# Kernel tuning notes

Hardware: AMD Instinct MI355X
Metric: run time of the kernel (lower is better)

## Reference

```python
import jax, jax.numpy as jnp
import numpy as np

N, IN_DIM, H, L, NH, LAT = 4096, 16, 128, 4, 8, 16
HD = H // NH
FF = 2 * H
DR_THR = 0.2
LN_EPS = 1e-5


def _ln(x, s, b):
    m = x.mean(-1, keepdims=True)
    v = ((x - m) ** 2).mean(-1, keepdims=True)
    return (x - m) * jax.lax.rsqrt(v + LN_EPS) * s + b


def compute_dr_mask(x_raw):
    eta = x_raw[:, 1] * (2.62 - (-2.62)) + (-2.62)
    phi = x_raw[:, 2] * (3.1416 - (-3.1416)) + (-3.1416)
    deta = eta[:, None] - eta[None, :]
    dphi = phi[:, None] - phi[None, :]
    dphi = jnp.arctan2(jnp.sin(dphi), jnp.cos(dphi))
    dr = jnp.sqrt(deta ** 2 + dphi ** 2)
    return jnp.where(dr <= DR_THR, 0.0, -jnp.inf).astype(jnp.float32)


def setup_inputs() -> dict:
    key = jax.random.key(0)
    ks = jax.random.split(key, 32)
    g = lambda i, shape, s=0.02: (jax.random.normal(ks[i], shape, dtype=jnp.float32) * s)
    inp = {
        'x_raw': jax.random.uniform(ks[0], (N, IN_DIM), dtype=jnp.float32),
        'batch': jnp.zeros((N,), dtype=jnp.int64) if jax.config.read('jax_enable_x64') else jnp.zeros((N,), dtype=jnp.int32),
        'in_w': g(1, (H, IN_DIM), 0.1), 'in_b': jnp.zeros((H,), jnp.float32),
        'ln1_s': jnp.ones((L, H), jnp.float32), 'ln1_b': jnp.zeros((L, H), jnp.float32),
        'qkv_w': g(2, (L, 3 * H, H)), 'qkv_b': jnp.zeros((L, 3 * H), jnp.float32),
        'ao_w': g(3, (L, H, H)), 'ao_b': jnp.zeros((L, H), jnp.float32),
        'ln2_s': jnp.ones((L, H), jnp.float32), 'ln2_b': jnp.zeros((L, H), jnp.float32),
        'f1_w': g(4, (L, FF, H)), 'f1_b': jnp.zeros((L, FF), jnp.float32),
        'f2_w': g(5, (L, H, FF)), 'f2_b': jnp.zeros((L, H), jnp.float32),
        'lat1_w': g(6, (H, H), 0.08), 'lat1_b': jnp.zeros((H,), jnp.float32),
        'lat2_w': g(7, (LAT, H), 0.08), 'lat2_b': jnp.zeros((LAT,), jnp.float32),
        'b1_w': g(8, (H // 2, H), 0.08), 'b1_b': jnp.zeros((H // 2,), jnp.float32),
        'b2_w': g(9, (1, H // 2), 0.008), 'b2_b': jnp.full((1,), -3.0, jnp.float32),
    }
    return inp


def reference(x_raw, batch, in_w, in_b, ln1_s, ln1_b, qkv_w, qkv_b, ao_w, ao_b,
              ln2_s, ln2_b, f1_w, f1_b, f2_w, f2_b,
              lat1_w, lat1_b, lat2_w, lat2_b, b1_w, b1_b, b2_w, b2_b):
    mask = jax.lax.stop_gradient(compute_dr_mask(x_raw))  # [N, N] additive mask
    x = x_raw @ in_w.T + in_b  # [N, H]
    scale = 1.0 / jnp.sqrt(jnp.float32(HD))
    for l in range(L):  # norm_first TransformerEncoderLayer, eval mode (no dropout)
        h = _ln(x, ln1_s[l], ln1_b[l])
        qkv = h @ qkv_w[l].T + qkv_b[l]
        q, k, v = [t.reshape(N, NH, HD) for t in jnp.split(qkv, 3, axis=-1)]
        scores = jnp.einsum('qhd,khd->hqk', q, k) * scale + mask[None]
        attn = jax.nn.softmax(scores, axis=-1)
        o = jnp.einsum('hqk,khd->qhd', attn, v).reshape(N, H)
        x = x + o @ ao_w[l].T + ao_b[l]
        h2 = _ln(x, ln2_s[l], ln2_b[l])
        x = x + jax.nn.relu(h2 @ f1_w[l].T + f1_b[l]) @ f2_w[l].T + f2_b[l]
    lat = jax.nn.relu(x @ lat1_w.T + lat1_b) @ lat2_w.T + lat2_b  # [N, LAT]
    lat = lat / jnp.maximum(jnp.linalg.norm(lat, axis=-1, keepdims=True), 1e-12)
    beta = jax.nn.sigmoid(jax.nn.relu(x @ b1_w.T + b1_b) @ b2_w.T + b2_b)
    beta = jnp.clip(beta, 1e-6, 1 - 1e-6)  # [N, 1]
    return beta, lat
```

## Files before the change

kernel.cpp:

```cpp
#include <hip/hip_runtime.h>
#include <hip/hip_bf16.h>

typedef unsigned short u16;
typedef short short8_t __attribute__((ext_vector_type(8)));
typedef float floatx4 __attribute__((ext_vector_type(4)));

constexpr int NT = 4096, H = 128, CAP = 64;
constexpr int GRID = 256, BLK = 512, GSTRIDE = GRID * BLK;

constexpr int OFF_QKV  = 0;
constexpr int OFF_AO   = 196608;
constexpr int OFF_F1   = 262144;
constexpr int OFF_F2   = 393216;
constexpr int OFF_LAT1 = 524288;
constexpr int OFF_B1   = 540672;
constexpr int OFF_LAT2 = 548864;
constexpr int W_TOTAL  = 550912;

__device__ __forceinline__ float bfu(u16 u) { return __uint_as_float(((unsigned)u) << 16); }
__device__ __forceinline__ u16 f2bf(float f) {
  unsigned u = __float_as_uint(f);
  u += 0x7fffu + ((u >> 16) & 1u);
  return (u16)(u >> 16);
}
__device__ __forceinline__ void unpack8(uint4 u, float* f) {
  f[0] = __uint_as_float(u.x << 16); f[1] = __uint_as_float(u.x & 0xffff0000u);
  f[2] = __uint_as_float(u.y << 16); f[3] = __uint_as_float(u.y & 0xffff0000u);
  f[4] = __uint_as_float(u.z << 16); f[5] = __uint_as_float(u.z & 0xffff0000u);
  f[6] = __uint_as_float(u.w << 16); f[7] = __uint_as_float(u.w & 0xffff0000u);
}
__device__ __forceinline__ short8_t cvt8(const float* bp) {
  const float4 f0 = *(const float4*)bp, f1 = *(const float4*)(bp + 4);
  short8_t r;
  r[0] = (short)f2bf(f0.x); r[1] = (short)f2bf(f0.y);
  r[2] = (short)f2bf(f0.z); r[3] = (short)f2bf(f0.w);
  r[4] = (short)f2bf(f1.x); r[5] = (short)f2bf(f1.y);
  r[6] = (short)f2bf(f1.z); r[7] = (short)f2bf(f1.w);
  return r;
}

struct Prm {
  const float *xr, *in_w, *in_b, *ln1_s, *ln1_b, *qkv_w, *qkv_b, *ao_w, *ao_b,
              *ln2_s, *ln2_b, *f1_w, *f1_b, *f2_w, *f2_b, *lat1_w, *lat1_b,
              *lat2_w, *lat2_b, *b1_w, *b1_b, *b2_w, *b2_b;
  u16* W; u16* QKV0; u16* QKV1; float* Xg; int* NI; int* NC; float* out;
};

__global__ __launch_bounds__(BLK, 2) void prep_kernel(Prm p) {
  const int t = threadIdx.x, bid = blockIdx.x;
  const int lane = t & 63, w = t >> 6;
  const int lr = lane & 15, quad = lane >> 4;
  const int gtid = bid * BLK + t;
  const int r0 = bid * 16;
  const floatx4 FZ = {0.f, 0.f, 0.f, 0.f};

  __shared__ float Xs[16][132];
  __shared__ union {
    unsigned long long words[8][64];
    struct { u16 A16[16][152]; } g;
    u16 QS[16][384];
  } sm;

  for (int i = 49152 + gtid; i < W_TOTAL; i += GSTRIDE) {
    float v;
    if      (i < OFF_AO)   v = p.qkv_w[i];
    else if (i < OFF_F1)   v = p.ao_w[i - OFF_AO];
    else if (i < OFF_F2)   v = p.f1_w[i - OFF_F1];
    else if (i < OFF_LAT1) v = p.f2_w[i - OFF_F2];
    else if (i < OFF_B1)   v = p.lat1_w[i - OFF_LAT1];
    else if (i < OFF_LAT2) v = p.b1_w[i - OFF_B1];
    else                   v = p.lat2_w[i - OFF_LAT2];
    p.W[i] = f2bf(v);
  }
  for (int i = t; i < 16 * H; i += BLK) {
    const int r = i >> 7, c = i & 127;
    const float* xp = p.xr + (size_t)(r0 + r) * 16;
    const float* wp = p.in_w + c * 16;
    float acc = p.in_b[c];
#pragma unroll
    for (int k = 0; k < 16; ++k) acc += xp[k] * wp[k];
    Xs[r][c] = acc;
    p.Xg[(size_t)(r0 + r) * H + c] = acc;
  }
  for (int uu = 0; uu < 2; ++uu) {
    const int q0 = r0 + uu * 8;
    double qe[8], qp_[8];
#pragma unroll
    for (int j = 0; j < 8; ++j) {
      qe[j]  = (double)p.xr[(q0 + j) * 16 + 1] * 5.24 - 2.62;
      qp_[j] = (double)p.xr[(q0 + j) * 16 + 2] * 6.2832 - 3.1416;
    }
    for (int c = 0; c < 8; ++c) {
      const int k = c * 512 + t;
      const double ke = (double)p.xr[k * 16 + 1] * 5.24 - 2.62;
      const double kp = (double)p.xr[k * 16 + 2] * 6.2832 - 3.1416;
#pragma unroll
      for (int j = 0; j < 8; ++j) {
        const double de = qe[j] - ke;
        double dp = qp_[j] - kp;
        dp -= 6.283185307179586 * rint(dp * 0.15915494309189535);
        const unsigned long long bm = __ballot((de * de + dp * dp) <= 0.04);
        if (lane == 0) sm.words[j][c * 8 + w] = bm;
      }
    }
    __syncthreads();
    {
      unsigned long long m = sm.words[w][lane];
      const int cnt = __popcll(m);
      int incl = cnt;
#pragma unroll
      for (int off = 1; off < 64; off <<= 1) {
        const int n = __shfl_up(incl, off);
        if (lane >= off) incl += n;
      }
      int pos = incl - cnt;
      const int qq = q0 + w;
      const int kbase = (lane >> 3) * 512 + (lane & 7) * 64;
      while (m) {
        const int b = __builtin_ctzll(m);
        m &= m - 1;
        if (pos < CAP) p.NI[qq * CAP + pos] = kbase + b;
        ++pos;
      }
      if (lane == 63) p.NC[qq] = incl > CAP ? CAP : incl;
    }
    __syncthreads();
  }
  {
    const int r = t >> 5, j0 = (t & 31) * 4;
    const float4 xv = *(const float4*)&Xs[r][j0];
    float v0 = xv.x, v1 = xv.y, v2 = xv.z, v3 = xv.w;
    float s = v0 + v1 + v2 + v3;
    float ss = v0 * v0 + v1 * v1 + v2 * v2 + v3 * v3;
#pragma unroll
    for (int off = 1; off <= 16; off <<= 1) {
      s += __shfl_xor(s, off); ss += __shfl_xor(ss, off);
    }
    const float mean = s * (1.f / 128.f);
    const float rstd = rsqrtf(ss * (1.f / 128.f) - mean * mean + 1e-5f);
    v0 = (v0 - mean) * rstd * p.ln1_s[j0]     + p.ln1_b[j0];
    v1 = (v1 - mean) * rstd * p.ln1_s[j0 + 1] + p.ln1_b[j0 + 1];
    v2 = (v2 - mean) * rstd * p.ln1_s[j0 + 2] + p.ln1_b[j0 + 2];
    v3 = (v3 - mean) * rstd * p.ln1_s[j0 + 3] + p.ln1_b[j0 + 3];
    uint2 pk;
    pk.x = (unsigned)f2bf(v0) | ((unsigned)f2bf(v1) << 16);
    pk.y = (unsigned)f2bf(v2) | ((unsigned)f2bf(v3) << 16);
    *(uint2*)&sm.g.A16[r][j0] = pk;
  }
  __syncthreads();
  {
    const int c0 = w * 48;
    floatx4 a0 = FZ, a1 = FZ, a2 = FZ;
#pragma unroll
    for (int k0 = 0; k0 < 128; k0 += 32) {
      short8_t a  = *(const short8_t*)&sm.g.A16[lr][k0 + quad * 8];
      short8_t b0 = cvt8(&p.qkv_w[(size_t)(c0 + lr) * 128 + k0 + quad * 8]);
      short8_t b1 = cvt8(&p.qkv_w[(size_t)(c0 + 16 + lr) * 128 + k0 + quad * 8]);
      short8_t b2 = cvt8(&p.qkv_w[(size_t)(c0 + 32 + lr) * 128 + k0 + quad * 8]);
      a0 = __builtin_amdgcn_mfma_f32_16x16x32_bf16(a, b0, a0, 0, 0, 0);
      a1 = __builtin_amdgcn_mfma_f32_16x16x32_bf16(a, b1, a1, 0, 0, 0);
      a2 = __builtin_amdgcn_mfma_f32_16x16x32_bf16(a, b2, a2, 0, 0, 0);
    }
    __syncthreads();
#pragma unroll
    for (int r = 0; r < 4; ++r) {
      const int row = quad * 4 + r;
      sm.QS[row][c0 + lr]      = f2bf(a0[r] + p.qkv_b[c0 + lr]);
      sm.QS[row][c0 + 16 + lr] = f2bf(a1[r] + p.qkv_b[c0 + 16 + lr]);
      sm.QS[row][c0 + 32 + lr] = f2bf(a2[r] + p.qkv_b[c0 + 32 + lr]);
    }
    __syncthreads();
    unsigned long long* d64 = (unsigned long long*)(p.QKV0 + (size_t)r0 * 384);
    const unsigned long long* s64 = (const unsigned long long*)&sm.QS[0][0];
    for (int j = t; j < 1536; j += BLK) d64[j] = s64[j];
  }
}

__global__ __launch_bounds__(BLK, 2) void layer_kernel(Prm p, int l,
                                                       const u16* __restrict__ qsrc,
                                                       u16* __restrict__ qdst) {
  const int t = threadIdx.x, bid = blockIdx.x;
  const int lane = t & 63, w = t >> 6;
  const int lr = lane & 15, quad = lane >> 4;
  const int r0 = bid * 16;
  const floatx4 FZ = {0.f, 0.f, 0.f, 0.f};

  __shared__ float Xs[16][132];
  __shared__ int NIs[16][CAP];
  __shared__ int NCs[16];
  __shared__ union {
    struct { u16 A16[16][152]; u16 FF1[16][280]; } g;
    u16 QS[16][384];
  } sm;

  {
    const int r = t >> 5, j0 = (t & 31) * 4;
    *(float4*)&Xs[r][j0] = *(const float4*)&p.Xg[(size_t)(r0 + r) * H + j0];
    for (int j = t; j < 16 * CAP; j += BLK) (&NIs[0][0])[j] = p.NI[r0 * CAP + j];
    if (t < 16) NCs[t] = p.NC[r0 + t];
  }

  auto stage_x = [&](const float* sc, const float* bi, bool do_ln) {
    const int r = t >> 5, j0 = (t & 31) * 4;
    const float4 xv = *(const float4*)&Xs[r][j0];
    float v0 = xv.x, v1 = xv.y, v2 = xv.z, v3 = xv.w;
    if (do_ln) {
      float s = v0 + v1 + v2 + v3;
      float ss = v0 * v0 + v1 * v1 + v2 * v2 + v3 * v3;
#pragma unroll
      for (int off = 1; off <= 16; off <<= 1) {
        s += __shfl_xor(s, off); ss += __shfl_xor(ss, off);
      }
      const float mean = s * (1.f / 128.f);
      const float rstd = rsqrtf(ss * (1.f / 128.f) - mean * mean + 1e-5f);
      v0 = (v0 - mean) * rstd * sc[j0]     + bi[j0];
      v1 = (v1 - mean) * rstd * sc[j0 + 1] + bi[j0 + 1];
      v2 = (v2 - mean) * rstd * sc[j0 + 2] + bi[j0 + 2];
      v3 = (v3 - mean) * rstd * sc[j0 + 3] + bi[j0 + 3];
    }
    uint2 pk;
    pk.x = (unsigned)f2bf(v0) | ((unsigned)f2bf(v1) << 16);
    pk.y = (unsigned)f2bf(v2) | ((unsigned)f2bf(v3) << 16);
    *(uint2*)&sm.g.A16[r][j0] = pk;
  };
  __syncthreads();

  {
    const int pr = t >> 2, sub = t & 3;
    const int lq = pr >> 3, h = pr & 7;
    const u16* qp = qsrc + (size_t)(r0 + lq) * 384 + h * 16;
    float qv[16];
    { uint4 a = *(const uint4*)qp, b = *(const uint4*)(qp + 8);
      unpack8(a, qv); unpack8(b, qv + 8); }
#pragma unroll
    for (int d = 0; d < 16; ++d) qv[d] *= 0.25f;
    float o[16];
#pragma unroll
    for (int d = 0; d < 16; ++d) o[d] = 0.f;
    float se = 0.f;
    const int cnt = NCs[lq];
    for (int i = sub; i < cnt; i += 4) {
      const int nb = NIs[lq][i];
      const u16* kp = qsrc + (size_t)nb * 384 + 128 + h * 16;
      float kv[16], vv[16];
      { uint4 a = *(const uint4*)kp;         uint4 b = *(const uint4*)(kp + 8);
        unpack8(a, kv); unpack8(b, kv + 8); }
      { uint4 a = *(const uint4*)(kp + 128); uint4 b = *(const uint4*)(kp + 136);
        unpack8(a, vv); unpack8(b, vv + 8); }
      float s0 = 0.f, s1 = 0.f, s2 = 0.f, s3 = 0.f;
#pragma unroll
      for (int d = 0; d < 16; d += 4) {
        s0 += qv[d] * kv[d];         s1 += qv[d + 1] * kv[d + 1];
        s2 += qv[d + 2] * kv[d + 2]; s3 += qv[d + 3] * kv[d + 3];
      }
      const float e = expf((s0 + s1) + (s2 + s3));
      se += e;
#pragma unroll
      for (int d = 0; d < 16; ++d) o[d] += e * vv[d];
    }
#pragma unroll
    for (int d = 0; d < 16; ++d) o[d] += __shfl_xor(o[d], 1);
    se += __shfl_xor(se, 1);
#pragma unroll
    for (int d = 0; d < 16; ++d) o[d] += __shfl_xor(o[d], 2);
    se += __shfl_xor(se, 2);
    if (sub == 0) {
      const float inv = 1.f / se;
      uint4 w0, w1;
      w0.x = (unsigned)f2bf(o[0] * inv)  | ((unsigned)f2bf(o[1] * inv) << 16);
      w0.y = (unsigned)f2bf(o[2] * inv)  | ((unsigned)f2bf(o[3] * inv) << 16);
      w0.z = (unsigned)f2bf(o[4] * inv)  | ((unsigned)f2bf(o[5] * inv) << 16);
      w0.w = (unsigned)f2bf(o[6] * inv)  | ((unsigned)f2bf(o[7] * inv) << 16);
      w1.x = (unsigned)f2bf(o[8] * inv)  | ((unsigned)f2bf(o[9] * inv) << 16);
      w1.y = (unsigned)f2bf(o[10] * inv) | ((unsigned)f2bf(o[11] * inv) << 16);
      w1.z = (unsigned)f2bf(o[12] * inv) | ((unsigned)f2bf(o[13] * inv) << 16);
      w1.w = (unsigned)f2bf(o[14] * inv) | ((unsigned)f2bf(o[15] * inv) << 16);
      *(uint4*)&sm.g.A16[lq][h * 16]     = w0;
      *(uint4*)&sm.g.A16[lq][h * 16 + 8] = w1;
    }
  }
  __syncthreads();
  {
    const u16* Bw = p.W + OFF_AO + l * 16384;
    const float* ab = p.ao_b + l * 128;
    const int col = w * 16 + lr;
    floatx4 acc = FZ;
#pragma unroll
    for (int k0 = 0; k0 < 128; k0 += 32) {
      short8_t a = *(const short8_t*)&sm.g.A16[lr][k0 + quad * 8];
      short8_t b = *(const short8_t*)&Bw[(size_t)col * 128 + k0 + quad * 8];
      acc = __builtin_amdgcn_mfma_f32_16x16x32_bf16(a, b, acc, 0, 0, 0);
    }
    const float bv = ab[col];
#pragma unroll
    for (int r = 0; r < 4; ++r)
      Xs[quad * 4 + r][col] += acc[r] + bv;
  }
  __syncthreads();
  stage_x(p.ln2_s + l * 128, p.ln2_b + l * 128, true);
  __syncthreads();
  {
    const u16* Bw = p.W + OFF_F1 + l * 32768;
    const float* fb = p.f1_b + l * 256;
    const int c0 = w * 32;
    floatx4 a0 = FZ, a1 = FZ;
#pragma unroll
    for (int k0 = 0; k0 < 128; k0 += 32) {
      short8_t a  = *(const short8_t*)&sm.g.A16[lr][k0 + quad * 8];
      short8_t b0 = *(const short8_t*)&Bw[(size_t)(c0 + lr) * 128 + k0 + quad * 8];
      short8_t b1 = *(const short8_t*)&Bw[(size_t)(c0 + 16 + lr) * 128 + k0 + quad * 8];
      a0 = __builtin_amdgcn_mfma_f32_16x16x32_bf16(a, b0, a0, 0, 0, 0);
      a1 = __builtin_amdgcn_mfma_f32_16x16x32_bf16(a, b1, a1, 0, 0, 0);
    }
#pragma unroll
    for (int r = 0; r < 4; ++r) {
      const int row = quad * 4 + r;
      sm.g.FF1[row][c0 + lr]      = f2bf(fmaxf(a0[r] + fb[c0 + lr], 0.f));
      sm.g.FF1[row][c0 + 16 + lr] = f2bf(fmaxf(a1[r] + fb[c0 + 16 + lr], 0.f));
    }
  }
  __syncthreads();
  {
    const u16* Bw = p.W + OFF_F2 + l * 32768;
    const float* fb = p.f2_b + l * 128;
    const int col = w * 16 + lr;
    floatx4 acc = FZ;
#pragma unroll
    for (int k0 = 0; k0 < 256; k0 += 32) {
      short8_t a = *(const short8_t*)&sm.g.FF1[lr][k0 + quad * 8];
      short8_t b = *(const short8_t*)&Bw[(size_t)col * 256 + k0 + quad * 8];
      acc = __builtin_amdgcn_mfma_f32_16x16x32_bf16(a, b, acc, 0, 0, 0);
    }
    const float bv = fb[col];
#pragma unroll
    for (int r = 0; r < 4; ++r)
      Xs[quad * 4 + r][col] += acc[r] + bv;
  }
  __syncthreads();
  if (l < 3) {
    {
      const int r = t >> 5, j0 = (t & 31) * 4;
      *(float4*)&p.Xg[(size_t)(r0 + r) * H + j0] = *(const float4*)&Xs[r][j0];
    }
    stage_x(p.ln1_s + (l + 1) * 128, p.ln1_b + (l + 1) * 128, true);
    __syncthreads();
    {
      const u16* Bw = p.W + OFF_QKV + (l + 1) * 49152;
      const float* qb = p.qkv_b + (l + 1) * 384;
      const int c0 = w * 48;
      floatx4 a0 = FZ, a1 = FZ, a2 = FZ;
#pragma unroll
      for (int k0 = 0; k0 < 128; k0 += 32) {
        short8_t a  = *(const short8_t*)&sm.g.A16[lr][k0 + quad * 8];
        short8_t b0 = *(const short8_t*)&Bw[(size_t)(c0 + lr) * 128 + k0 + quad * 8];
        short8_t b1 = *(const short8_t*)&Bw[(size_t)(c0 + 16 + lr) * 128 + k0 + quad * 8];
        short8_t b2 = *(const short8_t*)&Bw[(size_t)(c0 + 32 + lr) * 128 + k0 + quad * 8];
        a0 = __builtin_amdgcn_mfma_f32_16x16x32_bf16(a, b0, a0, 0, 0, 0);
        a1 = __builtin_amdgcn_mfma_f32_16x16x32_bf16(a, b1, a1, 0, 0, 0);
        a2 = __builtin_amdgcn_mfma_f32_16x16x32_bf16(a, b2, a2, 0, 0, 0);
      }
      __syncthreads();
#pragma unroll
      for (int r = 0; r < 4; ++r) {
        const int row = quad * 4 + r;
        sm.QS[row][c0 + lr]      = f2bf(a0[r] + qb[c0 + lr]);
        sm.QS[row][c0 + 16 + lr] = f2bf(a1[r] + qb[c0 + 16 + lr]);
        sm.QS[row][c0 + 32 + lr] = f2bf(a2[r] + qb[c0 + 32 + lr]);
      }
      __syncthreads();
      unsigned long long* d64 = (unsigned long long*)(qdst + (size_t)r0 * 384);
      const unsigned long long* s64 = (const unsigned long long*)&sm.QS[0][0];
      for (int j = t; j < 1536; j += BLK) d64[j] = s64[j];
    }
  } else {
    stage_x(nullptr, nullptr, false);
    __syncthreads();
    {
      const int c0 = w * 32;
      if (c0 < 192) {
        const u16* Bw = p.W + OFF_LAT1;
        floatx4 a0 = FZ, a1 = FZ;
#pragma unroll
        for (int k0 = 0; k0 < 128; k0 += 32) {
          short8_t a  = *(const short8_t*)&sm.g.A16[lr][k0 + quad * 8];
          short8_t b0 = *(const short8_t*)&Bw[(size_t)(c0 + lr) * 128 + k0 + quad * 8];
          short8_t b1 = *(const short8_t*)&Bw[(size_t)(c0 + 16 + lr) * 128 + k0 + quad * 8];
          a0 = __builtin_amdgcn_mfma_f32_16x16x32_bf16(a, b0, a0, 0, 0, 0);
          a1 = __builtin_amdgcn_mfma_f32_16x16x32_bf16(a, b1, a1, 0, 0, 0);
        }
        const int cA = c0 + lr, cB = c0 + 16 + lr;
        const float bA = cA < 128 ? p.lat1_b[cA] : p.b1_b[cA - 128];
        const float bB = cB < 128 ? p.lat1_b[cB] : p.b1_b[cB - 128];
#pragma unroll
        for (int r = 0; r < 4; ++r) {
          const int row = quad * 4 + r;
          sm.g.FF1[row][cA] = f2bf(fmaxf(a0[r] + bA, 0.f));
          sm.g.FF1[row][cB] = f2bf(fmaxf(a1[r] + bB, 0.f));
        }
      }
    }
    __syncthreads();
    if (t < 256) {
      const int r = t >> 4, c = t & 15;
      float acc = p.lat2_b[c];
      const u16* gw = p.W + OFF_LAT2 + c * 128;
      for (int k = 0; k < 128; ++k) acc += bfu(sm.g.FF1[r][k]) * bfu(gw[k]);
      float ss = acc * acc;
      ss += __shfl_xor(ss, 1); ss += __shfl_xor(ss, 2);
      ss += __shfl_xor(ss, 4); ss += __shfl_xor(ss, 8);
      p.out[NT + (size_t)(r0 + r) * 16 + c] = acc / fmaxf(sqrtf(ss), 1e-12f);
      float v = 0.f;
#pragma unroll
      for (int i = 0; i < 4; ++i)
        v += bfu(sm.g.FF1[r][128 + c * 4 + i]) * p.b2_w[c * 4 + i];
      v += __shfl_xor(v, 1); v += __shfl_xor(v, 2);
      v += __shfl_xor(v, 4); v += __shfl_xor(v, 8);
      if (c == 0) {
        v += p.b2_b[0];
        const float beta = 1.f / (1.f + expf(-v));
        p.out[r0 + r] = fminf(fmaxf(beta, 1e-6f), 1.f - 1e-6f);
      }
    }
  }
}

extern "C" void kernel_launch(void* const* d_in, const int* in_sizes, int n_in,
                              void* d_out, int out_size, void* d_ws, size_t ws_size,
                              hipStream_t stream) {
  Prm prm;
  prm.xr    = (const float*)d_in[0];
  prm.in_w  = (const float*)d_in[2];  prm.in_b  = (const float*)d_in[3];
  prm.ln1_s = (const float*)d_in[4];  prm.ln1_b = (const float*)d_in[5];
  prm.qkv_w = (const float*)d_in[6];  prm.qkv_b = (const float*)d_in[7];
  prm.ao_w  = (const float*)d_in[8];  prm.ao_b  = (const float*)d_in[9];
  prm.ln2_s = (const float*)d_in[10]; prm.ln2_b = (const float*)d_in[11];
  prm.f1_w  = (const float*)d_in[12]; prm.f1_b  = (const float*)d_in[13];
  prm.f2_w  = (const float*)d_in[14]; prm.f2_b  = (const float*)d_in[15];
  prm.lat1_w= (const float*)d_in[16]; prm.lat1_b= (const float*)d_in[17];
  prm.lat2_w= (const float*)d_in[18]; prm.lat2_b= (const float*)d_in[19];
  prm.b1_w  = (const float*)d_in[20]; prm.b1_b  = (const float*)d_in[21];
  prm.b2_w  = (const float*)d_in[22]; prm.b2_b  = (const float*)d_in[23];
  prm.out   = (float*)d_out;

  char* pw = (char*)d_ws;
  prm.W    = (u16*)pw;   pw += ((size_t)W_TOTAL * 2 + 255) & ~(size_t)255;
  prm.QKV0 = (u16*)pw;   pw += (size_t)NT * 384 * 2;
  prm.QKV1 = (u16*)pw;   pw += (size_t)NT * 384 * 2;
  prm.Xg   = (float*)pw; pw += (size_t)NT * H * 4;
  prm.NI   = (int*)pw;   pw += (size_t)NT * CAP * 4;
  prm.NC   = (int*)pw;   pw += (size_t)NT * 4;

  prep_kernel<<<GRID, BLK, 0, stream>>>(prm);
  layer_kernel<<<GRID, BLK, 0, stream>>>(prm, 0, prm.QKV0, prm.QKV1);
  layer_kernel<<<GRID, BLK, 0, stream>>>(prm, 1, prm.QKV1, prm.QKV0);
  layer_kernel<<<GRID, BLK, 0, stream>>>(prm, 2, prm.QKV0, prm.QKV1);
  layer_kernel<<<GRID, BLK, 0, stream>>>(prm, 3, prm.QKV1, nullptr);
}
```

Measured before the change: 198.3 us.

## Double block size to 1024 threads and redistribute work across 16 waves

Raises the block from 512 to 1024 threads (16 waves) at the same 16 rows per block, and remaps every stage to the extra waves. The stages affected are the mask ballot, the LayerNorm staging (one wave per row), the QKV, FF1 and lat1 MFMA column splits, and the neighbour attention, which now uses 8 sub-lanes per (query, head) instead of 4. The aim is more parallelism and latency hiding per block in the latency-bound attention gather. In exchange, launch bounds drop to one block per CU, some waves idle in the AO/F2 stages, and wave work is uneven in the QKV split.

```diff
diff --git a/kernel.cpp b/kernel.cpp
--- a/kernel.cpp
+++ b/kernel.cpp
@@ -2,11 +2,13 @@
 #include <hip/hip_bf16.h>
 
 typedef unsigned short u16;
+typedef unsigned long long u64;
 typedef short short8_t __attribute__((ext_vector_type(8)));
 typedef float floatx4 __attribute__((ext_vector_type(4)));
 
 constexpr int NT = 4096, H = 128, CAP = 64;
-constexpr int GRID = 256, BLK = 512, GSTRIDE = GRID * BLK;
+constexpr int GRID = 256, BLK = 1024, GSTRIDE = GRID * BLK;
+constexpr int ROWS = 16;
 
 constexpr int OFF_QKV  = 0;
 constexpr int OFF_AO   = 196608;
@@ -46,19 +48,19 @@
   u16* W; u16* QKV0; u16* QKV1; float* Xg; int* NI; int* NC; float* out;
 };
 
-__global__ __launch_bounds__(BLK, 2) void prep_kernel(Prm p) {
+__global__ __launch_bounds__(BLK, 1) void prep_kernel(Prm p) {
   const int t = threadIdx.x, bid = blockIdx.x;
   const int lane = t & 63, w = t >> 6;
   const int lr = lane & 15, quad = lane >> 4;
   const int gtid = bid * BLK + t;
-  const int r0 = bid * 16;
+  const int r0 = bid * ROWS;
   const floatx4 FZ = {0.f, 0.f, 0.f, 0.f};
 
-  __shared__ float Xs[16][132];
+  __shared__ float Xs[ROWS][132];
   __shared__ union {
     unsigned long long words[8][64];
-    struct { u16 A16[16][152]; } g;
-    u16 QS[16][384];
+    struct { u16 A16[ROWS][152]; } g;
+    u16 QS[ROWS][384];
   } sm;
 
   for (int i = 49152 + gtid; i < W_TOTAL; i += GSTRIDE) {
@@ -72,7 +74,7 @@
     else                   v = p.lat2_w[i - OFF_LAT2];
     p.W[i] = f2bf(v);
   }
-  for (int i = t; i < 16 * H; i += BLK) {
+  for (int i = t; i < ROWS * H; i += BLK) {
     const int r = i >> 7, c = i & 127;
     const float* xp = p.xr + (size_t)(r0 + r) * 16;
     const float* wp = p.in_w + c * 16;
@@ -90,8 +92,8 @@
       qe[j]  = (double)p.xr[(q0 + j) * 16 + 1] * 5.24 - 2.62;
       qp_[j] = (double)p.xr[(q0 + j) * 16 + 2] * 6.2832 - 3.1416;
     }
-    for (int c = 0; c < 8; ++c) {
-      const int k = c * 512 + t;
+    for (int c = 0; c < 4; ++c) {
+      const int k = c * 1024 + t;
       const double ke = (double)p.xr[k * 16 + 1] * 5.24 - 2.62;
       const double kp = (double)p.xr[k * 16 + 2] * 6.2832 - 3.1416;
 #pragma unroll
@@ -100,11 +102,11 @@
         double dp = qp_[j] - kp;
         dp -= 6.283185307179586 * rint(dp * 0.15915494309189535);
         const unsigned long long bm = __ballot((de * de + dp * dp) <= 0.04);
-        if (lane == 0) sm.words[j][c * 8 + w] = bm;
-      }
-    }
-    __syncthreads();
-    {
+        if (lane == 0) sm.words[j][c * 16 + w] = bm;
+      }
+    }
+    __syncthreads();
+    if (w < 8) {
       unsigned long long m = sm.words[w][lane];
       const int cnt = __popcll(m);
       int incl = cnt;
@@ -115,7 +117,7 @@
       }
       int pos = incl - cnt;
       const int qq = q0 + w;
-      const int kbase = (lane >> 3) * 512 + (lane & 7) * 64;
+      const int kbase = lane * 64;
       while (m) {
         const int b = __builtin_ctzll(m);
         m &= m - 1;
@@ -127,106 +129,92 @@
     __syncthreads();
   }
   {
-    const int r = t >> 5, j0 = (t & 31) * 4;
-    const float4 xv = *(const float4*)&Xs[r][j0];
-    float v0 = xv.x, v1 = xv.y, v2 = xv.z, v3 = xv.w;
-    float s = v0 + v1 + v2 + v3;
-    float ss = v0 * v0 + v1 * v1 + v2 * v2 + v3 * v3;
-#pragma unroll
-    for (int off = 1; off <= 16; off <<= 1) {
+    const int r = w, j0 = lane * 2;
+    float v0 = Xs[r][j0], v1 = Xs[r][j0 + 1];
+    float s = v0 + v1, ss = v0 * v0 + v1 * v1;
+#pragma unroll
+    for (int off = 1; off <= 32; off <<= 1) {
       s += __shfl_xor(s, off); ss += __shfl_xor(ss, off);
     }
     const float mean = s * (1.f / 128.f);
     const float rstd = rsqrtf(ss * (1.f / 128.f) - mean * mean + 1e-5f);
     v0 = (v0 - mean) * rstd * p.ln1_s[j0]     + p.ln1_b[j0];
     v1 = (v1 - mean) * rstd * p.ln1_s[j0 + 1] + p.ln1_b[j0 + 1];
-    v2 = (v2 - mean) * rstd * p.ln1_s[j0 + 2] + p.ln1_b[j0 + 2];
-    v3 = (v3 - mean) * rstd * p.ln1_s[j0 + 3] + p.ln1_b[j0 + 3];
-    uint2 pk;
-    pk.x = (unsigned)f2bf(v0) | ((unsigned)f2bf(v1) << 16);
-    pk.y = (unsigned)f2bf(v2) | ((unsigned)f2bf(v3) << 16);
-    *(uint2*)&sm.g.A16[r][j0] = pk;
+    *(unsigned*)&sm.g.A16[r][j0] = (unsigned)f2bf(v0) | ((unsigned)f2bf(v1) << 16);
   }
   __syncthreads();
   {
-    const int c0 = w * 48;
-    floatx4 a0 = FZ, a1 = FZ, a2 = FZ;
+    floatx4 a0 = FZ, a1 = FZ;
+    const int cA = (w < 8) ? (w * 32 + lr) : (256 + (w - 8) * 16 + lr);
+    const int cB = cA + 16;
 #pragma unroll
     for (int k0 = 0; k0 < 128; k0 += 32) {
       short8_t a  = *(const short8_t*)&sm.g.A16[lr][k0 + quad * 8];
-      short8_t b0 = cvt8(&p.qkv_w[(size_t)(c0 + lr) * 128 + k0 + quad * 8]);
-      short8_t b1 = cvt8(&p.qkv_w[(size_t)(c0 + 16 + lr) * 128 + k0 + quad * 8]);
-      short8_t b2 = cvt8(&p.qkv_w[(size_t)(c0 + 32 + lr) * 128 + k0 + quad * 8]);
+      short8_t b0 = cvt8(&p.qkv_w[(size_t)cA * 128 + k0 + quad * 8]);
       a0 = __builtin_amdgcn_mfma_f32_16x16x32_bf16(a, b0, a0, 0, 0, 0);
-      a1 = __builtin_amdgcn_mfma_f32_16x16x32_bf16(a, b1, a1, 0, 0, 0);
-      a2 = __builtin_amdgcn_mfma_f32_16x16x32_bf16(a, b2, a2, 0, 0, 0);
+      if (w < 8) {
+        short8_t b1 = cvt8(&p.qkv_w[(size_t)cB * 128 + k0 + quad * 8]);
+        a1 = __builtin_amdgcn_mfma_f32_16x16x32_bf16(a, b1, a1, 0, 0, 0);
+      }
     }
     __syncthreads();
 #pragma unroll
     for (int r = 0; r < 4; ++r) {
       const int row = quad * 4 + r;
-      sm.QS[row][c0 + lr]      = f2bf(a0[r] + p.qkv_b[c0 + lr]);
-      sm.QS[row][c0 + 16 + lr] = f2bf(a1[r] + p.qkv_b[c0 + 16 + lr]);
-      sm.QS[row][c0 + 32 + lr] = f2bf(a2[r] + p.qkv_b[c0 + 32 + lr]);
-    }
-    __syncthreads();
-    unsigned long long* d64 = (unsigned long long*)(p.QKV0 + (size_t)r0 * 384);
-    const unsigned long long* s64 = (const unsigned long long*)&sm.QS[0][0];
+      sm.QS[row][cA] = f2bf(a0[r] + p.qkv_b[cA]);
+      if (w < 8) sm.QS[row][cB] = f2bf(a1[r] + p.qkv_b[cB]);
+    }
+    __syncthreads();
+    u64* d64 = (u64*)(p.QKV0 + (size_t)r0 * 384);
+    const u64* s64 = (const u64*)&sm.QS[0][0];
     for (int j = t; j < 1536; j += BLK) d64[j] = s64[j];
   }
 }
 
-__global__ __launch_bounds__(BLK, 2) void layer_kernel(Prm p, int l,
+__global__ __launch_bounds__(BLK, 1) void layer_kernel(Prm p, int l,
                                                        const u16* __restrict__ qsrc,
                                                        u16* __restrict__ qdst) {
   const int t = threadIdx.x, bid = blockIdx.x;
   const int lane = t & 63, w = t >> 6;
   const int lr = lane & 15, quad = lane >> 4;
-  const int r0 = bid * 16;
+  const int r0 = bid * ROWS;
   const floatx4 FZ = {0.f, 0.f, 0.f, 0.f};
 
-  __shared__ float Xs[16][132];
-  __shared__ int NIs[16][CAP];
-  __shared__ int NCs[16];
+  __shared__ float Xs[ROWS][132];
+  __shared__ int NIs[ROWS][CAP];
+  __shared__ int NCs[ROWS];
   __shared__ union {
-    struct { u16 A16[16][152]; u16 FF1[16][280]; } g;
-    u16 QS[16][384];
+    struct { u16 A16[ROWS][152]; u16 FF1[ROWS][280]; } g;
+    u16 QS[ROWS][384];
   } sm;
 
   {
-    const int r = t >> 5, j0 = (t & 31) * 4;
-    *(float4*)&Xs[r][j0] = *(const float4*)&p.Xg[(size_t)(r0 + r) * H + j0];
-    for (int j = t; j < 16 * CAP; j += BLK) (&NIs[0][0])[j] = p.NI[r0 * CAP + j];
-    if (t < 16) NCs[t] = p.NC[r0 + t];
+    const int r = w, j0 = lane * 2;
+    *(float2*)&Xs[r][j0] = *(const float2*)&p.Xg[(size_t)(r0 + r) * H + j0];
+    if (t < ROWS * CAP) (&NIs[0][0])[t] = p.NI[r0 * CAP + t];
+    if (t < ROWS) NCs[t] = p.NC[r0 + t];
   }
 
   auto stage_x = [&](const float* sc, const float* bi, bool do_ln) {
-    const int r = t >> 5, j0 = (t & 31) * 4;
-    const float4 xv = *(const float4*)&Xs[r][j0];
-    float v0 = xv.x, v1 = xv.y, v2 = xv.z, v3 = xv.w;
+    const int r = w, j0 = lane * 2;
+    float v0 = Xs[r][j0], v1 = Xs[r][j0 + 1];
     if (do_ln) {
-      float s = v0 + v1 + v2 + v3;
-      float ss = v0 * v0 + v1 * v1 + v2 * v2 + v3 * v3;
-#pragma unroll
-      for (int off = 1; off <= 16; off <<= 1) {
+      float s = v0 + v1, ss = v0 * v0 + v1 * v1;
+#pragma unroll
+      for (int off = 1; off <= 32; off <<= 1) {
         s += __shfl_xor(s, off); ss += __shfl_xor(ss, off);
       }
       const float mean = s * (1.f / 128.f);
       const float rstd = rsqrtf(ss * (1.f / 128.f) - mean * mean + 1e-5f);
       v0 = (v0 - mean) * rstd * sc[j0]     + bi[j0];
       v1 = (v1 - mean) * rstd * sc[j0 + 1] + bi[j0 + 1];
-      v2 = (v2 - mean) * rstd * sc[j0 + 2] + bi[j0 + 2];
-      v3 = (v3 - mean) * rstd * sc[j0 + 3] + bi[j0 + 3];
-    }
-    uint2 pk;
-    pk.x = (unsigned)f2bf(v0) | ((unsigned)f2bf(v1) << 16);
-    pk.y = (unsigned)f2bf(v2) | ((unsigned)f2bf(v3) << 16);
-    *(uint2*)&sm.g.A16[r][j0] = pk;
+    }
+    *(unsigned*)&sm.g.A16[r][j0] = (unsigned)f2bf(v0) | ((unsigned)f2bf(v1) << 16);
   };
   __syncthreads();
 
   {
-    const int pr = t >> 2, sub = t & 3;
+    const int pr = t >> 3, sub = t & 7;
     const int lq = pr >> 3, h = pr & 7;
     const u16* qp = qsrc + (size_t)(r0 + lq) * 384 + h * 16;
     float qv[16];
@@ -239,7 +227,7 @@
     for (int d = 0; d < 16; ++d) o[d] = 0.f;
     float se = 0.f;
     const int cnt = NCs[lq];
-    for (int i = sub; i < cnt; i += 4) {
+    for (int i = sub; i < cnt; i += 8) {
       const int nb = NIs[lq][i];
       const u16* kp = qsrc + (size_t)nb * 384 + 128 + h * 16;
       float kv[16], vv[16];
@@ -259,11 +247,11 @@
       for (int d = 0; d < 16; ++d) o[d] += e * vv[d];
     }
 #pragma unroll
-    for (int d = 0; d < 16; ++d) o[d] += __shfl_xor(o[d], 1);
-    se += __shfl_xor(se, 1);
-#pragma unroll
-    for (int d = 0; d < 16; ++d) o[d] += __shfl_xor(o[d], 2);
-    se += __shfl_xor(se, 2);
+    for (int off = 1; off <= 4; off <<= 1) {
+#pragma unroll
+      for (int d = 0; d < 16; ++d) o[d] += __shfl_xor(o[d], off);
+      se += __shfl_xor(se, off);
+    }
     if (sub == 0) {
       const float inv = 1.f / se;
       uint4 w0, w1;
@@ -280,7 +268,7 @@
     }
   }
   __syncthreads();
-  {
+  if (w < 8) {
     const u16* Bw = p.W + OFF_AO + l * 16384;
     const float* ab = p.ao_b + l * 128;
     const int col = w * 16 + lr;
@@ -302,25 +290,21 @@
   {
     const u16* Bw = p.W + OFF_F1 + l * 32768;
     const float* fb = p.f1_b + l * 256;
-    const int c0 = w * 32;
-    floatx4 a0 = FZ, a1 = FZ;
+    const int col = w * 16 + lr;
+    floatx4 acc = FZ;
 #pragma unroll
     for (int k0 = 0; k0 < 128; k0 += 32) {
-      short8_t a  = *(const short8_t*)&sm.g.A16[lr][k0 + quad * 8];
-      short8_t b0 = *(const short8_t*)&Bw[(size_t)(c0 + lr) * 128 + k0 + quad * 8];
-      short8_t b1 = *(const short8_t*)&Bw[(size_t)(c0 + 16 + lr) * 128 + k0 + quad * 8];
-      a0 = __builtin_amdgcn_mfma_f32_16x16x32_bf16(a, b0, a0, 0, 0, 0);
-      a1 = __builtin_amdgcn_mfma_f32_16x16x32_bf16(a, b1, a1, 0, 0, 0);
-    }
-#pragma unroll
-    for (int r = 0; r < 4; ++r) {
-      const int row = quad * 4 + r;
-      sm.g.FF1[row][c0 + lr]      = f2bf(fmaxf(a0[r] + fb[c0 + lr], 0.f));
-      sm.g.FF1[row][c0 + 16 + lr] = f2bf(fmaxf(a1[r] + fb[c0 + 16 + lr], 0.f));
-    }
-  }
-  __syncthreads();
-  {
+      short8_t a = *(const short8_t*)&sm.g.A16[lr][k0 + quad * 8];
+      short8_t b = *(const short8_t*)&Bw[(size_t)col * 128 + k0 + quad * 8];
+      acc = __builtin_amdgcn_mfma_f32_16x16x32_bf16(a, b, acc, 0, 0, 0);
+    }
+    const float bv = fb[col];
+#pragma unroll
+    for (int r = 0; r < 4; ++r)
+      sm.g.FF1[quad * 4 + r][col] = f2bf(fmaxf(acc[r] + bv, 0.f));
+  }
+  __syncthreads();
+  if (w < 8) {
     const u16* Bw = p.W + OFF_F2 + l * 32768;
     const float* fb = p.f2_b + l * 128;
     const int col = w * 16 + lr;
@@ -339,65 +323,56 @@
   __syncthreads();
   if (l < 3) {
     {
-      const int r = t >> 5, j0 = (t & 31) * 4;
-      *(float4*)&p.Xg[(size_t)(r0 + r) * H + j0] = *(const float4*)&Xs[r][j0];
+      const int r = w, j0 = lane * 2;
+      *(float2*)&p.Xg[(size_t)(r0 + r) * H + j0] = *(const float2*)&Xs[r][j0];
     }
     stage_x(p.ln1_s + (l + 1) * 128, p.ln1_b + (l + 1) * 128, true);
     __syncthreads();
     {
       const u16* Bw = p.W + OFF_QKV + (l + 1) * 49152;
       const float* qb = p.qkv_b + (l + 1) * 384;
-      const int c0 = w * 48;
-      floatx4 a0 = FZ, a1 = FZ, a2 = FZ;
+      floatx4 a0 = FZ, a1 = FZ;
+      const int cA = (w < 8) ? (w * 32 + lr) : (256 + (w - 8) * 16 + lr);
+      const int cB = cA + 16;
 #pragma unroll
       for (int k0 = 0; k0 < 128; k0 += 32) {
         short8_t a  = *(const short8_t*)&sm.g.A16[lr][k0 + quad * 8];
-        short8_t b0 = *(const short8_t*)&Bw[(size_t)(c0 + lr) * 128 + k0 + quad * 8];
-        short8_t b1 = *(const short8_t*)&Bw[(size_t)(c0 + 16 + lr) * 128 + k0 + quad * 8];
-        short8_t b2 = *(const short8_t*)&Bw[(size_t)(c0 + 32 + lr) * 128 + k0 + quad * 8];
+        short8_t b0 = *(const short8_t*)&Bw[(size_t)cA * 128 + k0 + quad * 8];
         a0 = __builtin_amdgcn_mfma_f32_16x16x32_bf16(a, b0, a0, 0, 0, 0);
-        a1 = __builtin_amdgcn_mfma_f32_16x16x32_bf16(a, b1, a1, 0, 0, 0);
-        a2 = __builtin_amdgcn_mfma_f32_16x16x32_bf16(a, b2, a2, 0, 0, 0);
+        if (w < 8) {
+          short8_t b1 = *(const short8_t*)&Bw[(size_t)cB * 128 + k0 + quad * 8];
+          a1 = __builtin_amdgcn_mfma_f32_16x16x32_bf16(a, b1, a1, 0, 0, 0);
+        }
       }
       __syncthreads();
 #pragma unroll
       for (int r = 0; r < 4; ++r) {
         const int row = quad * 4 + r;
-        sm.QS[row][c0 + lr]      = f2bf(a0[r] + qb[c0 + lr]);
-        sm.QS[row][c0 + 16 + lr] = f2bf(a1[r] + qb[c0 + 16 + lr]);
-        sm.QS[row][c0 + 32 + lr] = f2bf(a2[r] + qb[c0 + 32 + lr]);
+        sm.QS[row][cA] = f2bf(a0[r] + qb[cA]);
+        if (w < 8) sm.QS[row][cB] = f2bf(a1[r] + qb[cB]);
       }
       __syncthreads();
-      unsigned long long* d64 = (unsigned long long*)(qdst + (size_t)r0 * 384);
-      const unsigned long long* s64 = (const unsigned long long*)&sm.QS[0][0];
+      u64* d64 = (u64*)(qdst + (size_t)r0 * 384);
+      const u64* s64 = (const u64*)&sm.QS[0][0];
       for (int j = t; j < 1536; j += BLK) d64[j] = s64[j];
     }
   } else {
     stage_x(nullptr, nullptr, false);
     __syncthreads();
-    {
-      const int c0 = w * 32;
-      if (c0 < 192) {
-        const u16* Bw = p.W + OFF_LAT1;
-        floatx4 a0 = FZ, a1 = FZ;
-#pragma unroll
-        for (int k0 = 0; k0 < 128; k0 += 32) {
-          short8_t a  = *(const short8_t*)&sm.g.A16[lr][k0 + quad * 8];
-          short8_t b0 = *(const short8_t*)&Bw[(size_t)(c0 + lr) * 128 + k0 + quad * 8];
-          short8_t b1 = *(const short8_t*)&Bw[(size_t)(c0 + 16 + lr) * 128 + k0 + quad * 8];
-          a0 = __builtin_amdgcn_mfma_f32_16x16x32_bf16(a, b0, a0, 0, 0, 0);
-          a1 = __builtin_amdgcn_mfma_f32_16x16x32_bf16(a, b1, a1, 0, 0, 0);
-        }
-        const int cA = c0 + lr, cB = c0 + 16 + lr;
-        const float bA = cA < 128 ? p.lat1_b[cA] : p.b1_b[cA - 128];
-        const float bB = cB < 128 ? p.lat1_b[cB] : p.b1_b[cB - 128];
-#pragma unroll
-        for (int r = 0; r < 4; ++r) {
-          const int row = quad * 4 + r;
-          sm.g.FF1[row][cA] = f2bf(fmaxf(a0[r] + bA, 0.f));
-          sm.g.FF1[row][cB] = f2bf(fmaxf(a1[r] + bB, 0.f));
-        }
-      }
+    if (w < 12) {
+      const u16* Bw = p.W + OFF_LAT1;
+      const int col = w * 16 + lr;
+      floatx4 acc = FZ;
+#pragma unroll
+      for (int k0 = 0; k0 < 128; k0 += 32) {
+        short8_t a = *(const short8_t*)&sm.g.A16[lr][k0 + quad * 8];
+        short8_t b = *(const short8_t*)&Bw[(size_t)col * 128 + k0 + quad * 8];
+        acc = __builtin_amdgcn_mfma_f32_16x16x32_bf16(a, b, acc, 0, 0, 0);
+      }
+      const float bv = col < 128 ? p.lat1_b[col] : p.b1_b[col - 128];
+#pragma unroll
+      for (int r = 0; r < 4; ++r)
+        sm.g.FF1[quad * 4 + r][col] = f2bf(fmaxf(acc[r] + bv, 0.f));
     }
     __syncthreads();
     if (t < 256) {
```

Measured after the change: 201.7 us. About the same (+1.7%).
